# Performance work log

Measured on AMD Instinct MI355X. Metric: run time of the kernel, lower is better.

The kernel has to match this reference:

```python
import jax, jax.numpy as jnp
import numpy as np

B, T, C, H = 4, 4096, 1024, 64


def setup_inputs() -> dict:
    key = jax.random.key(0)
    k1, k2, k3, k4 = jax.random.split(key, 4)
    x = jax.random.normal(k1, (B, T, C), dtype=jnp.float32)
    # nn.Linear(C, H, bias=False) weights, stored as [C, H] so y = x @ W
    Wq = jax.random.normal(k2, (C, H), dtype=jnp.float32) * (C ** -0.5)
    Wk = jax.random.normal(k3, (C, H), dtype=jnp.float32) * (C ** -0.5)
    Wv = jax.random.normal(k4, (C, H), dtype=jnp.float32) * (C ** -0.5)
    return {"x": x, "Wq": Wq, "Wk": Wk, "Wv": Wv}


def reference(x, Wq, Wk, Wv):
    # x: (B,T,C) -> q,k,v: (B,T,H)
    q = jnp.einsum('btc,ch->bth', x, Wq)
    k = jnp.einsum('btc,ch->bth', x, Wk)
    v = jnp.einsum('btc,ch->bth', x, Wv)
    scale = q.shape[-1] ** -0.5
    # (B,T,T) attention scores with causal mask
    scores = jnp.einsum('bqh,bkh->bqk', q, k) * scale
    t = x.shape[1]
    causal = jnp.tril(jnp.ones((t, t), dtype=bool))
    scores = jnp.where(causal, scores, -jnp.inf)
    attn = jax.nn.softmax(scores, axis=-1)
    return jnp.einsum('bqk,bkh->bqh', attn, v)
```

## Files before the change

kernel.cpp:

```cpp
#include <hip/hip_runtime.h>

#define BATCH 4
#define SEQ   4096
#define CDIM  1024
#define HDIM  64

typedef __attribute__((ext_vector_type(8))) short bf16x8;
typedef __attribute__((ext_vector_type(4))) float f32x4;

#define WT_OFF  0
#define Q_OFF   (3 * HDIM * CDIM)
#define KF_OFF  (Q_OFF + BATCH * SEQ * HDIM)
#define VF_OFF  (KF_OFF + BATCH * SEQ * HDIM)

static __device__ __forceinline__ short f2bf(float f) {
  union { float f; unsigned u; } a; a.f = f;
  unsigned r = a.u + 0x7fffu + ((a.u >> 16) & 1u);
  return (short)(r >> 16);
}

static __device__ __forceinline__ unsigned cvtpk(float lo, float hi) {
  unsigned r;
  asm("v_cvt_pk_bf16_f32 %0, %1, %2" : "=v"(r) : "v"(lo), "v"(hi));
  return r;
}

static __device__ __forceinline__ bf16x8 ld8(const short* p) {
  return *(const bf16x8*)p;
}

static __device__ __forceinline__ void bar_lgkm() {
  asm volatile("s_waitcnt lgkmcnt(0)\n\ts_barrier" ::: "memory");
}

__global__ void wcvt_kernel(const float* __restrict__ wq, const float* __restrict__ wk,
                            const float* __restrict__ wv, short* __restrict__ wt2) {
  int idx = blockIdx.x * 256 + threadIdx.x;
  int m = idx >> 16;
  int f = idx & 65535;
  int k0g = f >> 11, hc = (f >> 9) & 3, lr = (f >> 5) & 15, lg = (f >> 3) & 3, j = f & 7;
  int c = k0g * 32 + lg * 8 + j, h = hc * 16 + lr;
  const float* w = (m == 0) ? wq : (m == 1) ? wk : wv;
  wt2[((k0g * 12 + m * 4 + hc) * 64 + lr * 4 + lg) * 8 + j] = f2bf(w[c * 64 + h]);
}

__global__ __launch_bounds__(768, 3) void proj_kernel(const float* __restrict__ x,
                                                      const short* __restrict__ wt2,
                                                      short* __restrict__ ws) {
  __shared__ short xph[2][64 * 256];
  __shared__ short k_lds[4][4][16][16];
  __shared__ short v_lds[4][4][16][16];

  int tid = threadIdx.x;
  int widx = tid >> 6, lane = tid & 63;
  int lr = lane & 15, lg = lane >> 4;
  int row0 = blockIdx.x * 64;
  int p = widx;
  int m = p >> 2, hcw = p & 3;
  bool stager = (tid < 512);

  int sr = tid >> 3, sc8 = tid & 7;
  const float* xsrc = x + (size_t)(row0 + sr) * CDIM + sc8 * 32;
  int sbase = sr * 512;
  int sxor = (sr & 7) << 4;

  int axor = (lr & 7) << 4;

  const short* bptr = wt2 + p * 512 + (lr * 4 + lg) * 8;

  f32x4 acc[4] = {};

#define PLOAD(RG, PH) do {                                                   \
    if (stager) {                                                            \
      _Pragma("unroll")                                                      \
      for (int q = 0; q < 8; ++q)                                            \
        RG[q] = *(const float4*)(xsrc + (PH) * 256 + q * 4);                 \
    }                                                                        \
    __builtin_amdgcn_sched_barrier(0);               \
  } while (0)

#define PSTORE(RG, BUF) do {                                                 \
    if (stager) {                                                            \
      char* bc_ = (char*)&xph[(BUF)][0];                                     \
      _Pragma("unroll")                                                      \
      for (int d = 0; d < 4; ++d) {                                          \
        union { unsigned u[4]; bf16x8 v; } o_;                               \
        o_.u[0] = cvtpk(RG[d * 2].x, RG[d * 2].y);                           \
        o_.u[1] = cvtpk(RG[d * 2].z, RG[d * 2].w);                           \
        o_.u[2] = cvtpk(RG[d * 2 + 1].x, RG[d * 2 + 1].y);                   \
        o_.u[3] = cvtpk(RG[d * 2 + 1].z, RG[d * 2 + 1].w);                   \
        *(bf16x8*)(bc_ + sbase + ((sc8 * 64 + d * 16) ^ sxor)) = o_.v;       \
      }                                                                      \
    }                                                                        \
  } while (0)

#define PCOMPUTE(BUF, PH) do {                                               \
    const char* bufc_ = (const char*)&xph[(BUF)][0];                         \
    _Pragma("unroll")                                                        \
    for (int kk = 0; kk < 8; ++kk) {                                         \
      int co_ = (kk * 64 + lg * 16) ^ axor;                                  \
      bf16x8 bf_ = ld8(bptr + ((PH) * 8 + kk) * 6144);                       \
      _Pragma("unroll")                                                      \
      for (int t = 0; t < 4; ++t) {                                          \
        bf16x8 af_ = *(const bf16x8*)(bufc_ + (t * 16 + lr) * 512 + co_);    \
        acc[t] = __builtin_amdgcn_mfma_f32_16x16x32_bf16(af_, bf_, acc[t], 0, 0, 0); \
      }                                                                      \
    }                                                                        \
  } while (0)

  float4 rgA[8], rgB[8], rgC[8];
  PLOAD(rgA, 0);
  PLOAD(rgB, 1);
  PSTORE(rgA, 0);
  bar_lgkm();

  PLOAD(rgC, 2); PCOMPUTE(0, 0); PSTORE(rgB, 1); bar_lgkm();
  PLOAD(rgA, 3); PCOMPUTE(1, 1); PSTORE(rgC, 0); bar_lgkm();
                 PCOMPUTE(0, 2); PSTORE(rgA, 1); bar_lgkm();
                 PCOMPUTE(1, 3);

  short* qs  = ws + Q_OFF;
  short* kfr = ws + KF_OFF;
  short* vfr = ws + VF_OFF;

  if (m == 0) {
#pragma unroll
    for (int rt = 0; rt < 4; ++rt) {
      int rbase = row0 + rt * 16;
#pragma unroll
      for (int reg = 0; reg < 4; ++reg)
        qs[(rbase + lg * 4 + reg) * 64 + hcw * 16 + lr] = f2bf(acc[rt][reg]);
    }
  } else if (m == 1) {
#pragma unroll
    for (int rt = 0; rt < 4; ++rt)
#pragma unroll
      for (int reg = 0; reg < 4; ++reg)
        k_lds[hcw][rt][lg * 4 + reg][lr] = f2bf(acc[rt][reg]);
    if (lane < 32) {
      int i0 = lane >> 1, f8 = (lane & 1) * 8;
#pragma unroll
      for (int rt = 0; rt < 4; ++rt) {
        int rbase = row0 + rt * 16;
        int b = rbase >> 12, tb = rbase & (SEQ - 1);
        int kb64 = tb >> 6, st = (tb >> 4) & 3;
        size_t kblk = ((((size_t)b * 64 + kb64) * 4 + st) * 2 + (hcw >> 1)) * 512;
        bf16x8 kv8 = *(const bf16x8*)(&k_lds[hcw][rt][i0][f8]);
        *(bf16x8*)(kfr + kblk + ((hcw & 1) * 2 + (f8 >> 3)) * 128 + i0 * 8) = kv8;
      }
    }
  } else {
#pragma unroll
    for (int rt = 0; rt < 4; ++rt)
#pragma unroll
      for (int reg = 0; reg < 4; ++reg)
        v_lds[hcw][rt][lr][lg * 4 + reg] = f2bf(acc[rt][reg]);
    if (lane < 32) {
      int i0 = lane >> 1, f8 = (lane & 1) * 8;
#pragma unroll
      for (int rt = 0; rt < 4; ++rt) {
        int rbase = row0 + rt * 16;
        int b = rbase >> 12, tb = rbase & (SEQ - 1);
        int kb64 = tb >> 6;
        size_t vblk = ((((size_t)b * 64 + kb64) * 2 + ((tb >> 5) & 1)) * 4 + hcw) * 512;
        bf16x8 vv8 = *(const bf16x8*)(&v_lds[hcw][rt][i0][f8]);
        *(bf16x8*)(vfr + vblk + (((tb & 16) + f8) >> 3) * 128 + i0 * 8) = vv8;
      }
    }
  }
}

__global__ __launch_bounds__(512, 4) void attn_kernel(const short* __restrict__ ws,
                                                      float* __restrict__ out) {
  __shared__ float p_o[8][4][4][64];
  __shared__ float p_l[8][4][64];
  __shared__ short plds[8][16][72];

  int widx = threadIdx.x >> 6, lane = threadIdx.x & 63;
  int lr = lane & 15, lg = lane >> 4;
  int g = blockIdx.x;

  const short* qs  = ws + Q_OFF;
  const short* kfr = ws + KF_OFF;
  const short* vfr = ws + VF_OFF;
  short* myp = &plds[widx][0][0];

  for (int tt = 0; tt < 2; ++tt) {
    int j = tt == 0 ? g : 1023 - g;
    int t16 = 255 - (j >> 2), b = j & 3;
    int qrow0 = b * SEQ + t16 * 16;
    int nkv = (t16 >> 2) + 1;

    bf16x8 qf0 = ld8(qs + (qrow0 + lr) * 64 + lg * 8);
    bf16x8 qf1 = ld8(qs + (qrow0 + lr) * 64 + 32 + lg * 8);
    const short* kb_b = kfr + (size_t)b * 64 * 4096 + lane * 8;
    const short* vb_b = vfr + (size_t)b * 64 * 4096 + lane * 8;

    f32x4 o[4] = {};
    float l_run[4] = {};

    if (tt) __syncthreads();

    bf16x8 kf[8];
    int kvb = widx;
    if (kvb < nkv) {
      const short* kb = kb_b + (size_t)kvb * 4096;
#pragma unroll
      for (int q8 = 0; q8 < 8; ++q8) kf[q8] = ld8(kb + q8 * 512);
    }

    for (; kvb < nkv; kvb += 8) {
      int kv0 = kvb * 64;

      f32x4 s[4] = {};
#pragma unroll
      for (int st = 0; st < 4; ++st) {
        s[st] = __builtin_amdgcn_mfma_f32_16x16x32_bf16(qf0, kf[st * 2],     s[st], 0, 0, 0);
        s[st] = __builtin_amdgcn_mfma_f32_16x16x32_bf16(qf1, kf[st * 2 + 1], s[st], 0, 0, 0);
      }

      bf16x8 vv[8];
      {
        const short* vb = vb_b + (size_t)kvb * 4096;
#pragma unroll
        for (int q8 = 0; q8 < 8; ++q8) vv[q8] = ld8(vb + q8 * 512);
      }
      int kvn = kvb + 8;
      if (kvn < nkv) {
        const short* kb = kb_b + (size_t)kvn * 4096;
#pragma unroll
        for (int q8 = 0; q8 < 8; ++q8) kf[q8] = ld8(kb + q8 * 512);
      }

      bool last = (kvb == nkv - 1);
#pragma unroll
      for (int reg = 0; reg < 4; ++reg) {
        int ig = t16 * 16 + lg * 4 + reg;
#pragma unroll
        for (int st = 0; st < 4; ++st) {
          float v = s[st][reg] * 0.125f;
          if (last && (kv0 + st * 16 + lr > ig)) v = -1e30f;
          float p = __expf(v);
          l_run[reg] += p;
          myp[(lg * 4 + reg) * 72 + st * 16 + lr] = f2bf(p);
        }
      }
      asm volatile("s_waitcnt lgkmcnt(0)" ::: "memory");
      bf16x8 pf0 = ld8(myp + lr * 72 + lg * 8);
      bf16x8 pf1 = ld8(myp + lr * 72 + 32 + lg * 8);

#pragma unroll
      for (int hc = 0; hc < 4; ++hc) {
        o[hc] = __builtin_amdgcn_mfma_f32_16x16x32_bf16(pf0, vv[hc],     o[hc], 0, 0, 0);
        o[hc] = __builtin_amdgcn_mfma_f32_16x16x32_bf16(pf1, vv[4 + hc], o[hc], 0, 0, 0);
      }
    }

#pragma unroll
    for (int reg = 0; reg < 4; ++reg) {
      float l = l_run[reg];
      l += __shfl_xor(l, 1);
      l += __shfl_xor(l, 2);
      l += __shfl_xor(l, 4);
      l += __shfl_xor(l, 8);
      l_run[reg] = l;
    }

#pragma unroll
    for (int hc = 0; hc < 4; ++hc)
#pragma unroll
      for (int reg = 0; reg < 4; ++reg)
        p_o[widx][hc][reg][lane] = o[hc][reg];
#pragma unroll
    for (int reg = 0; reg < 4; ++reg)
      p_l[widx][reg][lane] = l_run[reg];
    __syncthreads();

    if (widx < 4) {
      int reg = widx;
      float lsum = 0.f;
#pragma unroll
      for (int w2 = 0; w2 < 8; ++w2) lsum += p_l[w2][reg][lane];
      float inv = 1.0f / lsum;
#pragma unroll
      for (int hc = 0; hc < 4; ++hc) {
        float sv = 0.f;
#pragma unroll
        for (int w2 = 0; w2 < 8; ++w2) sv += p_o[w2][hc][reg][lane];
        out[(qrow0 + lg * 4 + reg) * 64 + hc * 16 + lr] = sv * inv;
      }
    }
  }
}

extern "C" void kernel_launch(void* const* d_in, const int* in_sizes, int n_in,
                              void* d_out, int out_size, void* d_ws, size_t ws_size,
                              hipStream_t stream) {
  const float* x  = (const float*)d_in[0];
  const float* wq = (const float*)d_in[1];
  const float* wk = (const float*)d_in[2];
  const float* wv = (const float*)d_in[3];
  short* ws = (short*)d_ws;
  float* out = (float*)d_out;

  wcvt_kernel<<<dim3(768), dim3(256), 0, stream>>>(wq, wk, wv, ws + WT_OFF);
  proj_kernel<<<dim3(256), dim3(768), 0, stream>>>(x, ws + WT_OFF, ws);
  attn_kernel<<<dim3(512), dim3(512), 0, stream>>>(ws, out);
}
```

Baseline: 56.72 us.

## Compute transposed scores and pass P through lane shuffles instead of LDS

The QK^T MFMA now takes K as operand A, so each lane holds scores for kv positions rather than query rows. The bf16-packed probabilities are rearranged into the PV A-operand layout with cross-lane shuffles, which removes the per-wave LDS round trip and its waitcnt. The row-sum reduction is simplified to match, MFMA blocks are wrapped in s_setprio, and blocks are remapped so each XCD handles one batch for L2 locality. Launch-bounds occupancy drops from 4 to 3, and the shuffle-and-select sequence adds VALU work.

Result: slower. 58.43 us (median of 3 runs) (+3.0%).

```diff
diff --git a/kernel.cpp b/kernel.cpp
--- a/kernel.cpp
+++ b/kernel.cpp
@@ -63,9 +63,7 @@
   const float* xsrc = x + (size_t)(row0 + sr) * CDIM + sc8 * 32;
   int sbase = sr * 512;
   int sxor = (sr & 7) << 4;
-
   int axor = (lr & 7) << 4;
-
   const short* bptr = wt2 + p * 512 + (lr * 4 + lg) * 8;
 
   f32x4 acc[4] = {};
@@ -76,7 +74,7 @@
       for (int q = 0; q < 8; ++q)                                            \
         RG[q] = *(const float4*)(xsrc + (PH) * 256 + q * 4);                 \
     }                                                                        \
-    __builtin_amdgcn_sched_barrier(0);               \
+    __builtin_amdgcn_sched_barrier(0);                                       \
   } while (0)
 
 #define PSTORE(RG, BUF) do {                                                 \
@@ -170,26 +168,27 @@
   }
 }
 
-__global__ __launch_bounds__(512, 4) void attn_kernel(const short* __restrict__ ws,
+__global__ __launch_bounds__(512, 3) void attn_kernel(const short* __restrict__ ws,
                                                       float* __restrict__ out) {
   __shared__ float p_o[8][4][4][64];
-  __shared__ float p_l[8][4][64];
-  __shared__ short plds[8][16][72];
+  __shared__ float p_l[8][16];
 
   int widx = threadIdx.x >> 6, lane = threadIdx.x & 63;
   int lr = lane & 15, lg = lane >> 4;
   int g = blockIdx.x;
+  int xcd = g & 7;
+  int b = xcd & 3;
+  int i2 = (g >> 3) + ((xcd >> 2) << 6);
 
   const short* qs  = ws + Q_OFF;
   const short* kfr = ws + KF_OFF;
   const short* vfr = ws + VF_OFF;
-  short* myp = &plds[widx][0][0];
 
   for (int tt = 0; tt < 2; ++tt) {
-    int j = tt == 0 ? g : 1023 - g;
-    int t16 = 255 - (j >> 2), b = j & 3;
+    int t16 = tt == 0 ? 255 - i2 : i2;
     int qrow0 = b * SEQ + t16 * 16;
     int nkv = (t16 >> 2) + 1;
+    int qg = t16 * 16 + lr;
 
     bf16x8 qf0 = ld8(qs + (qrow0 + lr) * 64 + lg * 8);
     bf16x8 qf1 = ld8(qs + (qrow0 + lr) * 64 + 32 + lg * 8);
@@ -197,7 +196,7 @@
     const short* vb_b = vfr + (size_t)b * 64 * 4096 + lane * 8;
 
     f32x4 o[4] = {};
-    float l_run[4] = {};
+    float lsum = 0.f;
 
     if (tt) __syncthreads();
 
@@ -212,12 +211,14 @@
     for (; kvb < nkv; kvb += 8) {
       int kv0 = kvb * 64;
 
-      f32x4 s[4] = {};
+      f32x4 stx[4] = {};
+      __builtin_amdgcn_s_setprio(1);
 #pragma unroll
       for (int st = 0; st < 4; ++st) {
-        s[st] = __builtin_amdgcn_mfma_f32_16x16x32_bf16(qf0, kf[st * 2],     s[st], 0, 0, 0);
-        s[st] = __builtin_amdgcn_mfma_f32_16x16x32_bf16(qf1, kf[st * 2 + 1], s[st], 0, 0, 0);
-      }
+        stx[st] = __builtin_amdgcn_mfma_f32_16x16x32_bf16(kf[st * 2],     qf0, stx[st], 0, 0, 0);
+        stx[st] = __builtin_amdgcn_mfma_f32_16x16x32_bf16(kf[st * 2 + 1], qf1, stx[st], 0, 0, 0);
+      }
+      __builtin_amdgcn_s_setprio(0);
 
       bf16x8 vv[8];
       {
@@ -233,61 +234,89 @@
       }
 
       bool last = (kvb == nkv - 1);
+      float p[4][4];
+#pragma unroll
+      for (int st = 0; st < 4; ++st)
+#pragma unroll
+        for (int reg = 0; reg < 4; ++reg) {
+          int kvg = kv0 + st * 16 + lg * 4 + reg;
+          float v = stx[st][reg] * 0.125f;
+          if (last && kvg > qg) v = -1e30f;
+          float pv = __expf(v);
+          p[st][reg] = pv;
+          lsum += pv;
+        }
+
+      unsigned uu[4], uu2[4];
 #pragma unroll
       for (int reg = 0; reg < 4; ++reg) {
-        int ig = t16 * 16 + lg * 4 + reg;
-#pragma unroll
-        for (int st = 0; st < 4; ++st) {
-          float v = s[st][reg] * 0.125f;
-          if (last && (kv0 + st * 16 + lr > ig)) v = -1e30f;
-          float p = __expf(v);
-          l_run[reg] += p;
-          myp[(lg * 4 + reg) * 72 + st * 16 + lr] = f2bf(p);
-        }
-      }
-      asm volatile("s_waitcnt lgkmcnt(0)" ::: "memory");
-      bf16x8 pf0 = ld8(myp + lr * 72 + lg * 8);
-      bf16x8 pf1 = ld8(myp + lr * 72 + 32 + lg * 8);
-
+        uu[reg]  = cvtpk(p[0][reg], p[1][reg]);
+        uu2[reg] = cvtpk(p[2][reg], p[3][reg]);
+      }
+      int sl0 = lr + ((lg & 1) << 5);
+      int sl1 = sl0 + 16;
+      bool hi = (lg & 2) != 0;
+
+      unsigned a0 = (unsigned)__shfl((int)uu[0], sl0);
+      unsigned a1 = (unsigned)__shfl((int)uu[1], sl0);
+      unsigned a2 = (unsigned)__shfl((int)uu[2], sl0);
+      unsigned a3 = (unsigned)__shfl((int)uu[3], sl0);
+      unsigned a4 = (unsigned)__shfl((int)uu[0], sl1);
+      unsigned a5 = (unsigned)__shfl((int)uu[1], sl1);
+      unsigned a6 = (unsigned)__shfl((int)uu[2], sl1);
+      unsigned a7 = (unsigned)__shfl((int)uu[3], sl1);
+      union { unsigned u[4]; bf16x8 v; } pk0, pk1;
+      pk0.u[0] = hi ? ((a0 >> 16) | (a1 & 0xffff0000u)) : ((a0 & 0xffffu) | (a1 << 16));
+      pk0.u[1] = hi ? ((a2 >> 16) | (a3 & 0xffff0000u)) : ((a2 & 0xffffu) | (a3 << 16));
+      pk0.u[2] = hi ? ((a4 >> 16) | (a5 & 0xffff0000u)) : ((a4 & 0xffffu) | (a5 << 16));
+      pk0.u[3] = hi ? ((a6 >> 16) | (a7 & 0xffff0000u)) : ((a6 & 0xffffu) | (a7 << 16));
+
+      unsigned b0 = (unsigned)__shfl((int)uu2[0], sl0);
+      unsigned b1 = (unsigned)__shfl((int)uu2[1], sl0);
+      unsigned b2 = (unsigned)__shfl((int)uu2[2], sl0);
+      unsigned b3 = (unsigned)__shfl((int)uu2[3], sl0);
+      unsigned b4 = (unsigned)__shfl((int)uu2[0], sl1);
+      unsigned b5 = (unsigned)__shfl((int)uu2[1], sl1);
+      unsigned b6 = (unsigned)__shfl((int)uu2[2], sl1);
+      unsigned b7 = (unsigned)__shfl((int)uu2[3], sl1);
+      pk1.u[0] = hi ? ((b0 >> 16) | (b1 & 0xffff0000u)) : ((b0 & 0xffffu) | (b1 << 16));
+      pk1.u[1] = hi ? ((b2 >> 16) | (b3 & 0xffff0000u)) : ((b2 & 0xffffu) | (b3 << 16));
+      pk1.u[2] = hi ? ((b4 >> 16) | (b5 & 0xffff0000u)) : ((b4 & 0xffffu) | (b5 << 16));
+      pk1.u[3] = hi ? ((b6 >> 16) | (b7 & 0xffff0000u)) : ((b6 & 0xffffu) | (b7 << 16));
+
+      __builtin_amdgcn_s_setprio(1);
 #pragma unroll
       for (int hc = 0; hc < 4; ++hc) {
-        o[hc] = __builtin_amdgcn_mfma_f32_16x16x32_bf16(pf0, vv[hc],     o[hc], 0, 0, 0);
-        o[hc] = __builtin_amdgcn_mfma_f32_16x16x32_bf16(pf1, vv[4 + hc], o[hc], 0, 0, 0);
-      }
-    }
-
-#pragma unroll
-    for (int reg = 0; reg < 4; ++reg) {
-      float l = l_run[reg];
-      l += __shfl_xor(l, 1);
-      l += __shfl_xor(l, 2);
-      l += __shfl_xor(l, 4);
-      l += __shfl_xor(l, 8);
-      l_run[reg] = l;
-    }
+        o[hc] = __builtin_amdgcn_mfma_f32_16x16x32_bf16(pk0.v, vv[hc],     o[hc], 0, 0, 0);
+        o[hc] = __builtin_amdgcn_mfma_f32_16x16x32_bf16(pk1.v, vv[4 + hc], o[hc], 0, 0, 0);
+      }
+      __builtin_amdgcn_s_setprio(0);
+    }
+
+    lsum += __shfl_xor(lsum, 16);
+    lsum += __shfl_xor(lsum, 32);
 
 #pragma unroll
     for (int hc = 0; hc < 4; ++hc)
 #pragma unroll
       for (int reg = 0; reg < 4; ++reg)
         p_o[widx][hc][reg][lane] = o[hc][reg];
-#pragma unroll
-    for (int reg = 0; reg < 4; ++reg)
-      p_l[widx][reg][lane] = l_run[reg];
+    if (lg == 0) p_l[widx][lr] = lsum;
     __syncthreads();
 
     if (widx < 4) {
       int reg = widx;
-      float lsum = 0.f;
-#pragma unroll
-      for (int w2 = 0; w2 < 8; ++w2) lsum += p_l[w2][reg][lane];
-      float inv = 1.0f / lsum;
+      int q = lg * 4 + reg;
+      float L = 0.f;
+#pragma unroll
+      for (int w2 = 0; w2 < 8; ++w2) L += p_l[w2][q];
+      float inv = 1.0f / L;
 #pragma unroll
       for (int hc = 0; hc < 4; ++hc) {
         float sv = 0.f;
 #pragma unroll
         for (int w2 = 0; w2 < 8; ++w2) sv += p_o[w2][hc][reg][lane];
-        out[(qrow0 + lg * 4 + reg) * 64 + hc * 16 + lr] = sv * inv;
+        out[(qrow0 + q) * 64 + hc * 16 + lr] = sv * inv;
       }
     }
   }
```
